# Optimization experiments

Hardware: AMD Instinct MI355X
Metric: run time of the kernel (lower is better)

## Reference

```python
import jax, jax.numpy as jnp
import numpy as np

K = 16  # knn


def conv1x1(x, w, b):
    # x: (B,Cin,k,N), w: (Cout,Cin), b: (Cout,)
    return jnp.einsum('oc,bckn->bokn', w, x) + b[None, :, None, None]


def leaky(x):
    return jnp.where(x >= 0, x, 0.2 * x)


def conv_res(x, sc_w, sc_b, a_w, a_b, b_w, b_b, c_w, c_b):
    sc = conv1x1(x, sc_w, sc_b)
    h = leaky(conv1x1(x, a_w, a_b))
    h = leaky(conv1x1(h, b_w, b_b))
    h = conv1x1(h, c_w, c_b)
    return h + sc


def get_knn_feature(xyz, k):
    # xyz: (B,3,N) -> feature (B,10,k,N)
    x_t = jnp.transpose(xyz, (0, 2, 1))  # (B,N,3)
    xx = jnp.sum(x_t * x_t, axis=-1)  # (B,N)
    inner = jnp.einsum('bnc,bmc->bnm', x_t, x_t)  # (B,N,N)
    d2 = xx[:, :, None] + xx[:, None, :] - 2.0 * inner  # squared dists
    _, idx = jax.lax.top_k(-d2, k)  # (B,N,k) nearest (includes self)
    neighbors = jax.vmap(lambda pts, i: pts[i])(x_t, idx)  # (B,N,k,3)
    center = x_t[:, :, None, :]  # (B,N,1,3)
    rel = neighbors - center
    dist = jnp.sqrt(jnp.sum(rel * rel, axis=-1, keepdims=True) + 1e-12)  # (B,N,k,1)
    feat = jnp.concatenate([jnp.broadcast_to(center, neighbors.shape), neighbors, rel, dist], axis=-1)  # (B,N,k,10)
    return jnp.transpose(feat, (0, 3, 2, 1))  # (B,10,k,N)


def _mk_w(key, o, i):
    s = 1.0 / np.sqrt(i)
    return jax.random.uniform(key, (o, i), jnp.float32, -s, s)


def setup_inputs():
    key = jax.random.key(0)
    ks = jax.random.split(key, 20)
    B, N = 4, 8192
    hide, out = 64, 128
    inp = {'xyz': jax.random.normal(ks[0], (B, 3, N), jnp.float32)}
    # CONV_Res(10, 64, 64)
    inp['p1_sc_w'] = _mk_w(ks[1], hide, 10); inp['p1_sc_b'] = jnp.zeros((hide,), jnp.float32)
    inp['p1_a_w'] = _mk_w(ks[2], hide, 10); inp['p1_a_b'] = jnp.zeros((hide,), jnp.float32)
    inp['p1_b_w'] = _mk_w(ks[3], hide, hide); inp['p1_b_b'] = jnp.zeros((hide,), jnp.float32)
    inp['p1_c_w'] = _mk_w(ks[4], hide, hide); inp['p1_c_b'] = jnp.zeros((hide,), jnp.float32)
    # CONV_Res(128, 64, 128)
    inp['p2_sc_w'] = _mk_w(ks[5], out, 2 * hide); inp['p2_sc_b'] = jnp.zeros((out,), jnp.float32)
    inp['p2_a_w'] = _mk_w(ks[6], hide, 2 * hide); inp['p2_a_b'] = jnp.zeros((hide,), jnp.float32)
    inp['p2_b_w'] = _mk_w(ks[7], out, hide); inp['p2_b_b'] = jnp.zeros((out,), jnp.float32)
    inp['p2_c_w'] = _mk_w(ks[8], out, out); inp['p2_c_b'] = jnp.zeros((out,), jnp.float32)
    return inp


def reference(xyz, p1_sc_w, p1_sc_b, p1_a_w, p1_a_b, p1_b_w, p1_b_b, p1_c_w, p1_c_b,
              p2_sc_w, p2_sc_b, p2_a_w, p2_a_b, p2_b_w, p2_b_b, p2_c_w, p2_c_b):
    x = get_knn_feature(xyz, K)  # (B,10,k,N)
    x = conv_res(x, p1_sc_w, p1_sc_b, p1_a_w, p1_a_b, p1_b_w, p1_b_b, p1_c_w, p1_c_b)  # (B,64,k,N)
    x1 = jnp.max(x, axis=2, keepdims=True)  # (B,64,1,N)
    x1 = jnp.broadcast_to(x1, x.shape)  # repeat over k
    x = jnp.concatenate([x, x1], axis=1)  # (B,128,k,N)
    x = conv_res(x, p2_sc_w, p2_sc_b, p2_a_w, p2_a_b, p2_b_w, p2_b_b, p2_c_w, p2_c_b)  # (B,128,k,N)
    return jnp.max(x, axis=2)  # (B,128,N)
```

## Files before the change

kernel.cpp:

```cpp
#include <hip/hip_runtime.h>
#include <hip/hip_bf16.h>

#define B_ 4
#define N_ 8192
#define KNN 16
#define BN_ (B_*N_)
#define NPOS (BN_*KNN)

typedef __attribute__((ext_vector_type(8))) short bf16x8;
typedef __attribute__((ext_vector_type(4))) float f32x4;

static __device__ __forceinline__ unsigned short f2bf(float f) {
  union { float f; unsigned u; } v; v.f = f;
  unsigned r = v.u + 0x7fff + ((v.u >> 16) & 1);
  return (unsigned short)(r >> 16);
}
static __device__ __forceinline__ float lk(float x) { return x >= 0.f ? x : 0.2f*x; }
static __device__ __forceinline__ unsigned pk2(float a, float b) {
  return (unsigned)f2bf(a) | ((unsigned)f2bf(b) << 16);
}

__global__ void k_prep(const float* __restrict__ xyz, float4* __restrict__ pts4) {
  int i = blockIdx.x * 256 + threadIdx.x;
  if (i >= BN_) return;
  int b = i >> 13, n = i & (N_-1);
  const float* p = xyz + b*3*N_;
  float x = p[n], y = p[N_+n], z = p[2*N_+n];
  float xx = fmaf(z, z, fmaf(y, y, x*x));
  pts4[i] = make_float4(x, y, z, xx);
}

__global__ void k_wcvt(const float* __restrict__ w_sc, const float* __restrict__ w_a,
                       const float* __restrict__ w_b, const float* __restrict__ w_c,
                       const float* __restrict__ p1a, const float* __restrict__ p1sc,
                       const float* __restrict__ p1b, const float* __restrict__ p1c,
                       unsigned short* __restrict__ out) {
  int i = blockIdx.x*256 + threadIdx.x;
  if (i >= 61440) return;
  if (i < 49152) {
    int x = i*2;
    const float* w; int base, K2;
    if (x < 32768)      { w = w_sc; base = 0;     K2 = 256; }
    else if (x < 49152) { w = w_a;  base = 32768; K2 = 256; }
    else if (x < 65536) { w = w_b;  base = 49152; K2 = 128; }
    else                { w = w_c;  base = 65536; K2 = 256; }
    int off = x - base;
    int row = off / K2;
    int colb = (off & (K2-1)) ^ ((row & 7) << 4);
    int k = colb >> 1;
    out[i] = f2bf(w[row*(K2 >> 1) + k]);
  } else {
    int e = i - 49152;
    float val; int byteoff;
    if (e < 2048) {
      int row = e >> 5, k = e & 31;
      val = (k < 10) ? p1a[row*10 + k] : 0.f;
      byteoff = row*64 + ((2*k) ^ ((row & 3) << 4));
    } else if (e < 4096) {
      int le = e - 2048, row = le >> 5, k = le & 31;
      val = (k < 10) ? p1sc[row*10 + k] : 0.f;
      byteoff = 4096 + row*64 + ((2*k) ^ ((row & 3) << 4));
    } else if (e < 8192) {
      int le = e - 4096, row = le >> 6, k = le & 63;
      val = p1b[row*64 + k];
      byteoff = 8192 + row*128 + ((2*k) ^ ((row & 7) << 4));
    } else {
      int le = e - 8192, row = le >> 6, k = le & 63;
      val = p1c[row*64 + k];
      byteoff = 16384 + row*128 + ((2*k) ^ ((row & 7) << 4));
    }
    out[49152 + (byteoff >> 1)] = f2bf(val);
  }
}

static __device__ __forceinline__ unsigned long long bitonic64(
    unsigned long long key, int lane) {
  #pragma unroll
  for (int size = 2; size <= 64; size <<= 1) {
    #pragma unroll
    for (int stride = size >> 1; stride >= 1; stride >>= 1) {
      unsigned long long ok = __shfl_xor((long long)key, stride);
      bool up = ((lane & size) == 0);
      bool keepmin = (((lane & stride) == 0) == up);
      bool oless = ok < key;
      if (oless == keepmin) key = ok;
    }
  }
  return key;
}

template<int U>
static __device__ __forceinline__ void scan_groups(
    const float4* __restrict__ cand, int itbase, int ch,
    float4 me, int lane,
    unsigned long long* __restrict__ bw,
    unsigned long long& topk, float& rhs, int& cnt) {
  float s[U]; int cid[U];
  #pragma unroll
  for (int u = 0; u < U; ++u) {
    int ci = (itbase + u)*64 + lane;
    float4 c = cand[ci];
    float dot = fmaf(me.z, c.z, fmaf(me.y, c.y, me.x*c.x));
    s[u] = fmaf(-2.0f, dot, c.w);
    cid[u] = ch*2048 + ci;
  }
  #pragma unroll
  for (int u = 0; u < U; ++u) {
    unsigned long long m = __ballot(s[u] < rhs);
    if (m) {
      int prefix = __builtin_amdgcn_mbcnt_hi((unsigned)(m >> 32),
                    __builtin_amdgcn_mbcnt_lo((unsigned)m, 0));
      if (s[u] < rhs) {
        float d2 = me.w + s[u];
        bw[cnt + prefix] =
          ((unsigned long long)__float_as_uint(d2) << 32) | (unsigned)cid[u];
      }
      cnt += __popcll(m);
      if (cnt >= 48) {
        int base = 0;
        while (cnt > 0) {
          int c2 = cnt > 48 ? 48 : cnt;
          unsigned long long e = (lane < 16) ? topk
            : ((lane - 16) < c2 ? bw[base + lane - 16] : ~0ull);
          topk = bitonic64(e, lane);
          base += c2; cnt -= c2;
        }
        unsigned long long k15 = __shfl((long long)topk, 15);
        rhs = __uint_as_float((unsigned)(k15 >> 32)) - me.w;
      }
    }
  }
}

__global__ __launch_bounds__(512) void k_knn(const float4* __restrict__ pts4,
                                             int* __restrict__ knn) {
  __shared__ float4 cand[2048];
  __shared__ unsigned long long buf[8][112];
  const int lane = threadIdx.x & 63;
  const int wv   = threadIdx.x >> 6;
  const int q = blockIdx.x * 8 + wv;
  const int b = q >> 13;
  const int n = q & (N_-1);
  const float4* __restrict__ P = pts4 + (b << 13);
  float4 me = P[n];

  unsigned long long topk = ~0ull;
  float rhs = __builtin_inff();
  int cnt = 0;
  unsigned long long* __restrict__ bw = buf[wv];

  for (int ch = 0; ch < 4; ++ch) {
    __syncthreads();
    #pragma unroll
    for (int t = 0; t < 4; ++t)
      cand[t*512 + threadIdx.x] = P[ch*2048 + t*512 + threadIdx.x];
    __syncthreads();

    if (ch == 0) {
      float4 c = cand[lane];
      float dot = fmaf(me.z, c.z, fmaf(me.y, c.y, me.x*c.x));
      float d2 = (me.w + c.w) - 2.0f*dot;
      unsigned long long key =
        ((unsigned long long)__float_as_uint(d2) << 32) | (unsigned)lane;
      topk = bitonic64(key, lane);
      unsigned long long k15 = __shfl((long long)topk, 15);
      rhs = __uint_as_float((unsigned)(k15 >> 32)) - me.w;
      scan_groups<3>(cand, 1, 0, me, lane, bw, topk, rhs, cnt);
      #pragma unroll 1
      for (int it = 4; it < 32; it += 4)
        scan_groups<4>(cand, it, 0, me, lane, bw, topk, rhs, cnt);
    } else {
      #pragma unroll 1
      for (int it = 0; it < 32; it += 4)
        scan_groups<4>(cand, it, ch, me, lane, bw, topk, rhs, cnt);
    }
  }
  {
    int base = 0;
    while (cnt > 0) {
      int c2 = cnt > 48 ? 48 : cnt;
      unsigned long long e = (lane < 16) ? topk
        : ((lane - 16) < c2 ? bw[base + lane - 16] : ~0ull);
      topk = bitonic64(e, lane);
      base += c2; cnt -= c2;
    }
  }
  if (lane < 16) knn[(q << 4) + lane] = (int)(unsigned)(topk & 0xffffffffu);
}

__global__ __launch_bounds__(512, 4) void k_p1(
    const float4* __restrict__ pts4, const int* __restrict__ knn,
    const unsigned short* __restrict__ wbf,
    const float* __restrict__ a_b, const float* __restrict__ b_b,
    const float* __restrict__ c_b, const float* __restrict__ sc_b,
    unsigned short* __restrict__ X, unsigned short* __restrict__ XM) {
  __shared__ __align__(16) unsigned short Ws1[12288];
  __shared__ __align__(16) unsigned short Fs[8192];
  __shared__ __align__(16) unsigned short Hr[16384];
  const int tid = threadIdx.x;
  const int lane = tid & 63, wv = tid >> 6;
  const int colr = lane & 15, kq = lane >> 4;

  #pragma unroll
  for (int j = 0; j < 3; ++j) {
    int c = j*512 + tid;
    ((uint4*)Ws1)[c] = ((const uint4*)(wbf + 49152))[c];
  }
  const char* WS = (const char*)Ws1;
  char* H = (char*)Hr + wv*4096;

  for (int tile = 0; tile < 4; ++tile) {
    const int bn0 = (blockIdx.x*4 + tile) * 16;
    __syncthreads();
    if (tid < 256) {
      int bnl = tid >> 4, kk = tid & 15;
      int bn = bn0 + bnl;
      int b = bn >> 13;
      float4 cp = pts4[bn];
      int nid = knn[bn*16 + kk];
      float4 np = pts4[(b << 13) + nid];
      float rx = np.x - cp.x, ry = np.y - cp.y, rz = np.z - cp.z;
      float dist = sqrtf(fmaf(rz, rz, fmaf(ry, ry, rx*rx)) + 1e-12f);
      unsigned short row[32];
      row[0]=f2bf(cp.x); row[1]=f2bf(cp.y); row[2]=f2bf(cp.z);
      row[3]=f2bf(np.x); row[4]=f2bf(np.y); row[5]=f2bf(np.z);
      row[6]=f2bf(rx);   row[7]=f2bf(ry);   row[8]=f2bf(rz);   row[9]=f2bf(dist);
      #pragma unroll
      for (int j = 10; j < 32; ++j) row[j] = 0;
      int wvp = tid >> 5, posl = tid & 31;
      char* dst = (char*)Fs + wvp*2048 + posl*64;
      #pragma unroll
      for (int c = 0; c < 4; ++c)
        *(uint4*)(dst + ((c*16) ^ ((posl&3)<<4))) = *(const uint4*)(row + c*8);
    }
    __syncthreads();

    bf16x8 bfr[2];
    #pragma unroll
    for (int ct = 0; ct < 2; ++ct) {
      int posl = ct*16 + colr;
      bfr[ct] = *(const bf16x8*)((const char*)Fs + wv*2048 + posl*64 + ((kq*16) ^ ((posl&3)<<4)));
    }

    f32x4 acc[4][2];
    #pragma unroll
    for (int mt = 0; mt < 4; ++mt) {
      int r0 = mt*16 + kq*4;
      #pragma unroll
      for (int r = 0; r < 4; ++r) {
        float bia = c_b[r0+r] + sc_b[r0+r];
        acc[mt][0][r] = bia; acc[mt][1][r] = bia;
      }
    }
    #pragma unroll
    for (int mt = 0; mt < 4; ++mt) {
      int row = mt*16 + colr;
      bf16x8 w = *(const bf16x8*)(WS + 4096 + row*64 + ((kq*16) ^ ((row&3)<<4)));
      acc[mt][0] = __builtin_amdgcn_mfma_f32_16x16x32_bf16(w, bfr[0], acc[mt][0], 0, 0, 0);
      acc[mt][1] = __builtin_amdgcn_mfma_f32_16x16x32_bf16(w, bfr[1], acc[mt][1], 0, 0, 0);
    }

    f32x4 ha[4][2];
    #pragma unroll
    for (int mt = 0; mt < 4; ++mt) {
      int r0 = mt*16 + kq*4;
      #pragma unroll
      for (int r = 0; r < 4; ++r) { ha[mt][0][r] = a_b[r0+r]; ha[mt][1][r] = a_b[r0+r]; }
    }
    #pragma unroll
    for (int mt = 0; mt < 4; ++mt) {
      int row = mt*16 + colr;
      bf16x8 w = *(const bf16x8*)(WS + row*64 + ((kq*16) ^ ((row&3)<<4)));
      ha[mt][0] = __builtin_amdgcn_mfma_f32_16x16x32_bf16(w, bfr[0], ha[mt][0], 0, 0, 0);
      ha[mt][1] = __builtin_amdgcn_mfma_f32_16x16x32_bf16(w, bfr[1], ha[mt][1], 0, 0, 0);
    }

    #pragma unroll
    for (int mt = 0; mt < 4; ++mt) {
      int ch2 = (mt*16 + kq*4) * 2;
      #pragma unroll
      for (int ct = 0; ct < 2; ++ct) {
        int posl = ct*16 + colr;
        uint2 u;
        u.x = pk2(lk(ha[mt][ct][0]), lk(ha[mt][ct][1]));
        u.y = pk2(lk(ha[mt][ct][2]), lk(ha[mt][ct][3]));
        *(uint2*)(H + posl*128 + (ch2 ^ ((posl&7)<<4))) = u;
      }
    }
    bf16x8 bh[2][2];
    #pragma unroll
    for (int ct = 0; ct < 2; ++ct) {
      int posl = ct*16 + colr;
      #pragma unroll
      for (int k2 = 0; k2 < 2; ++k2)
        bh[ct][k2] = *(const bf16x8*)(H + posl*128 + ((k2*64 + kq*16) ^ ((posl&7)<<4)));
    }

    #pragma unroll
    for (int jj = 0; jj < 2; ++jj) {
      f32x4 h2[2][2];
      #pragma unroll
      for (int mtp = 0; mtp < 2; ++mtp) {
        int r0 = (jj*2 + mtp)*16 + kq*4;
        #pragma unroll
        for (int r = 0; r < 4; ++r) { h2[mtp][0][r] = b_b[r0+r]; h2[mtp][1][r] = b_b[r0+r]; }
      }
      #pragma unroll
      for (int mtp = 0; mtp < 2; ++mtp) {
        int row = (jj*2 + mtp)*16 + colr;
        #pragma unroll
        for (int k2 = 0; k2 < 2; ++k2) {
          bf16x8 w = *(const bf16x8*)(WS + 8192 + row*128 + ((k2*64 + kq*16) ^ ((row&7)<<4)));
          h2[mtp][0] = __builtin_amdgcn_mfma_f32_16x16x32_bf16(w, bh[0][k2], h2[mtp][0], 0, 0, 0);
          h2[mtp][1] = __builtin_amdgcn_mfma_f32_16x16x32_bf16(w, bh[1][k2], h2[mtp][1], 0, 0, 0);
        }
      }
      #pragma unroll
      for (int mtp = 0; mtp < 2; ++mtp) {
        int ch2 = ((jj*2 + mtp)*16 + kq*4) * 2;
        #pragma unroll
        for (int ct = 0; ct < 2; ++ct) {
          int posl = ct*16 + colr;
          uint2 u;
          u.x = pk2(lk(h2[mtp][ct][0]), lk(h2[mtp][ct][1]));
          u.y = pk2(lk(h2[mtp][ct][2]), lk(h2[mtp][ct][3]));
          *(uint2*)(H + posl*128 + (ch2 ^ ((posl&7)<<4))) = u;
        }
      }
      bf16x8 b2[2];
      #pragma unroll
      for (int ct = 0; ct < 2; ++ct) {
        int posl = ct*16 + colr;
        b2[ct] = *(const bf16x8*)(H + posl*128 + ((jj*64 + kq*16) ^ ((posl&7)<<4)));
      }
      #pragma unroll
      for (int mt = 0; mt < 4; ++mt) {
        int row = mt*16 + colr;
        bf16x8 w = *(const bf16x8*)(WS + 16384 + row*128 + ((jj*64 + kq*16) ^ ((row&7)<<4)));
        acc[mt][0] = __builtin_amdgcn_mfma_f32_16x16x32_bf16(w, b2[0], acc[mt][0], 0, 0, 0);
        acc[mt][1] = __builtin_amdgcn_mfma_f32_16x16x32_bf16(w, b2[1], acc[mt][1], 0, 0, 0);
      }
    }

    #pragma unroll
    for (int ct = 0; ct < 2; ++ct) {
      int bn = bn0 + wv*2 + ct;
      #pragma unroll
      for (int mt = 0; mt < 4; ++mt) {
        int ch0 = mt*16 + kq*4;
        uint2 u;
        u.x = pk2(acc[mt][ct][0], acc[mt][ct][1]);
        u.y = pk2(acc[mt][ct][2], acc[mt][ct][3]);
        *(uint2*)(X + ((size_t)(bn*16 + colr))*64 + ch0) = u;
        float m[4];
        #pragma unroll
        for (int r = 0; r < 4; ++r) {
          float v = acc[mt][ct][r];
          v = fmaxf(v, __shfl_xor(v, 1));
          v = fmaxf(v, __shfl_xor(v, 2));
          v = fmaxf(v, __shfl_xor(v, 4));
          v = fmaxf(v, __shfl_xor(v, 8));
          m[r] = v;
        }
        if (colr == 0) {
          uint2 um; um.x = pk2(m[0], m[1]); um.y = pk2(m[2], m[3]);
          *(uint2*)(XM + (size_t)bn*64 + ch0) = um;
        }
      }
    }
  }
}

struct P2Shared {
  unsigned short Ws[49152];
  unsigned short Hr[8][2048];
  float outT[128][16];
};

static __device__ __forceinline__ void p2_loadbx(
    bf16x8 (&dst)[2][4], const unsigned short* __restrict__ X,
    const unsigned short* __restrict__ XM, int bn0, int wv, int colr, int kq) {
  #pragma unroll
  for (int ct = 0; ct < 2; ++ct) {
    int bn = bn0 + wv*2 + ct;
    const unsigned short* xr = X + ((size_t)bn*16 + colr)*64 + kq*8;
    dst[ct][0] = *(const bf16x8*)(xr);
    dst[ct][1] = *(const bf16x8*)(xr + 32);
    const unsigned short* mr = XM + (size_t)bn*64 + kq*8;
    dst[ct][2] = *(const bf16x8*)(mr);
    dst[ct][3] = *(const bf16x8*)(mr + 32);
  }
}

__global__ __launch_bounds__(512, 2) void k_p2(
    const unsigned short* __restrict__ X, const unsigned short* __restrict__ XM,
    const unsigned short* __restrict__ wbf,
    const float* __restrict__ sc_b, const float* __restrict__ a_b,
    const float* __restrict__ b_b, const float* __restrict__ c_b,
    float* __restrict__ out) {
  __shared__ __align__(16) P2Shared S;
  const int tid = threadIdx.x;
  const int lane = tid & 63, wv = tid >> 6;
  const int colr = lane & 15, kq = lane >> 4;

  #pragma unroll
  for (int it = 0; it < 12; ++it) {
    int c = it*512 + tid;
    *(uint4*)((char*)S.Ws + c*16) = *(const uint4*)((const char*)wbf + c*16);
  }

  const char* WSC = (const char*)S.Ws;
  const char* WA  = (const char*)(S.Ws + 16384);
  const char* WB  = (const char*)(S.Ws + 24576);
  const char* WC  = (const char*)(S.Ws + 32768);
  char* H = (char*)S.Hr[wv];

#define WF(base, row, K2, ksbyte) \
  (*(const bf16x8*)((base) + (row)*(K2) + ((((ksbyte) + kq*16)) ^ (((row)&7)<<4))))

  bf16x8 bx[2][4], bxn[2][4];
  p2_loadbx(bx, X, XM, blockIdx.x*8*16, wv, colr, kq);
  __syncthreads();

  for (int t = 0; t < 8; ++t) {
    const int bn0 = (blockIdx.x*8 + t) * 16;

    f32x4 acc[8][2];
    #pragma unroll
    for (int mt = 0; mt < 8; ++mt) {
      int r0 = mt*16 + kq*4;
      #pragma unroll
      for (int r = 0; r < 4; ++r) {
        float bia = c_b[r0+r] + sc_b[r0+r];
        acc[mt][0][r] = bia; acc[mt][1][r] = bia;
      }
    }
    #pragma unroll
    for (int mt = 0; mt < 8; ++mt) {
      int row = mt*16 + colr;
      #pragma unroll
      for (int ks = 0; ks < 4; ++ks) {
        bf16x8 w = WF(WSC, row, 256, ks*64);
        acc[mt][0] = __builtin_amdgcn_mfma_f32_16x16x32_bf16(w, bx[0][ks], acc[mt][0], 0, 0, 0);
        acc[mt][1] = __builtin_amdgcn_mfma_f32_16x16x32_bf16(w, bx[1][ks], acc[mt][1], 0, 0, 0);
      }
    }

    f32x4 ha[4][2];
    #pragma unroll
    for (int mt = 0; mt < 4; ++mt) {
      int r0 = mt*16 + kq*4;
      #pragma unroll
      for (int r = 0; r < 4; ++r) { ha[mt][0][r] = a_b[r0+r]; ha[mt][1][r] = a_b[r0+r]; }
    }
    #pragma unroll
    for (int mt = 0; mt < 4; ++mt) {
      int row = mt*16 + colr;
      #pragma unroll
      for (int ks = 0; ks < 4; ++ks) {
        bf16x8 w = WF(WA, row, 256, ks*64);
        ha[mt][0] = __builtin_amdgcn_mfma_f32_16x16x32_bf16(w, bx[0][ks], ha[mt][0], 0, 0, 0);
        ha[mt][1] = __builtin_amdgcn_mfma_f32_16x16x32_bf16(w, bx[1][ks], ha[mt][1], 0, 0, 0);
      }
    }

    {
      int tn = (t < 7) ? (t + 1) : 7;
      p2_loadbx(bxn, X, XM, (blockIdx.x*8 + tn) * 16, wv, colr, kq);
    }

    #pragma unroll
    for (int mt = 0; mt < 4; ++mt) {
      int ch2 = (mt*16 + kq*4) * 2;
      #pragma unroll
      for (int ct = 0; ct < 2; ++ct) {
        int posl = ct*16 + colr;
        uint2 u;
        u.x = pk2(lk(ha[mt][ct][0]), lk(ha[mt][ct][1]));
        u.y = pk2(lk(ha[mt][ct][2]), lk(ha[mt][ct][3]));
        *(uint2*)(H + posl*128 + (ch2 ^ ((posl&7)<<4))) = u;
      }
    }
    bf16x8 bh[2][2];
    #pragma unroll
    for (int ct = 0; ct < 2; ++ct) {
      int posl = ct*16 + colr;
      #pragma unroll
      for (int k2 = 0; k2 < 2; ++k2)
        bh[ct][k2] = *(const bf16x8*)(H + posl*128 + ((k2*64 + kq*16) ^ ((posl&7)<<4)));
    }

    #pragma unroll
    for (int j = 0; j < 4; ++j) {
      f32x4 h2[2][2];
      #pragma unroll
      for (int mtp = 0; mtp < 2; ++mtp) {
        int r0 = (2*j + mtp)*16 + kq*4;
        #pragma unroll
        for (int r = 0; r < 4; ++r) { h2[mtp][0][r] = b_b[r0+r]; h2[mtp][1][r] = b_b[r0+r]; }
      }
      #pragma unroll
      for (int mtp = 0; mtp < 2; ++mtp) {
        int row = (2*j + mtp)*16 + colr;
        #pragma unroll
        for (int k2 = 0; k2 < 2; ++k2) {
          bf16x8 w = WF(WB, row, 128, k2*64);
          h2[mtp][0] = __builtin_amdgcn_mfma_f32_16x16x32_bf16(w, bh[0][k2], h2[mtp][0], 0, 0, 0);
          h2[mtp][1] = __builtin_amdgcn_mfma_f32_16x16x32_bf16(w, bh[1][k2], h2[mtp][1], 0, 0, 0);
        }
      }
      char* PB = H + (j & 1)*2048;
      #pragma unroll
      for (int mtp = 0; mtp < 2; ++mtp) {
        int chp2 = (mtp*16 + kq*4) * 2;
        #pragma unroll
        for (int ct = 0; ct < 2; ++ct) {
          int posl = ct*16 + colr;
          uint2 u;
          u.x = pk2(lk(h2[mtp][ct][0]), lk(h2[mtp][ct][1]));
          u.y = pk2(lk(h2[mtp][ct][2]), lk(h2[mtp][ct][3]));
          *(uint2*)(PB + posl*64 + (chp2 ^ ((posl&3)<<4))) = u;
        }
      }
      bf16x8 b2[2];
      #pragma unroll
      for (int ct = 0; ct < 2; ++ct) {
        int posl = ct*16 + colr;
        b2[ct] = *(const bf16x8*)(PB + posl*64 + ((kq*16) ^ ((posl&3)<<4)));
      }
      #pragma unroll
      for (int mt = 0; mt < 8; ++mt) {
        int row = mt*16 + colr;
        bf16x8 w = WF(WC, row, 256, j*64);
        acc[mt][0] = __builtin_amdgcn_mfma_f32_16x16x32_bf16(w, b2[0], acc[mt][0], 0, 0, 0);
        acc[mt][1] = __builtin_amdgcn_mfma_f32_16x16x32_bf16(w, b2[1], acc[mt][1], 0, 0, 0);
      }
    }

    __syncthreads();
    #pragma unroll
    for (int mt = 0; mt < 8; ++mt) {
      #pragma unroll
      for (int ct = 0; ct < 2; ++ct) {
        #pragma unroll
        for (int r = 0; r < 4; ++r) {
          float v = acc[mt][ct][r];
          v = fmaxf(v, __shfl_xor(v, 1));
          v = fmaxf(v, __shfl_xor(v, 2));
          v = fmaxf(v, __shfl_xor(v, 4));
          v = fmaxf(v, __shfl_xor(v, 8));
          if (colr == 0) S.outT[mt*16 + kq*4 + r][wv*2 + ct] = v;
        }
      }
    }
    __syncthreads();
    {
      int ch = tid >> 2, p = tid & 3;
      int b = bn0 >> 13, n0 = bn0 & (N_-1);
      float4 v4 = *(const float4*)&S.outT[ch][p*4];
      *(float4*)(out + ((size_t)b*128 + ch)*N_ + n0 + p*4) = v4;
    }

    #pragma unroll
    for (int ct = 0; ct < 2; ++ct)
      #pragma unroll
      for (int ks = 0; ks < 4; ++ks)
        bx[ct][ks] = bxn[ct][ks];
  }
#undef WF
}

extern "C" void kernel_launch(void* const* d_in, const int* in_sizes, int n_in,
                              void* d_out, int out_size, void* d_ws, size_t ws_size,
                              hipStream_t stream) {
  const float* xyz     = (const float*)d_in[0];
  const float* p1_sc_w = (const float*)d_in[1];
  const float* p1_sc_b = (const float*)d_in[2];
  const float* p1_a_w  = (const float*)d_in[3];
  const float* p1_a_b  = (const float*)d_in[4];
  const float* p1_b_w  = (const float*)d_in[5];
  const float* p1_b_b  = (const float*)d_in[6];
  const float* p1_c_w  = (const float*)d_in[7];
  const float* p1_c_b  = (const float*)d_in[8];
  const float* p2_sc_w = (const float*)d_in[9];
  const float* p2_sc_b = (const float*)d_in[10];
  const float* p2_a_w  = (const float*)d_in[11];
  const float* p2_a_b  = (const float*)d_in[12];
  const float* p2_b_w  = (const float*)d_in[13];
  const float* p2_b_b  = (const float*)d_in[14];
  const float* p2_c_w  = (const float*)d_in[15];
  const float* p2_c_b  = (const float*)d_in[16];

  if (ws_size < 75497472u) return;
  char* ws = (char*)d_ws;
  float4* pts4        = (float4*)(ws);
  unsigned short* wbf = (unsigned short*)(ws + 524288);
  int* knn            = (int*)(ws + 655360);
  unsigned short* X   = (unsigned short*)(ws + 4194304);
  unsigned short* XM  = (unsigned short*)(ws + 4194304 + 67108864);
  float* out = (float*)d_out;

  k_prep<<<dim3(BN_/256), dim3(256), 0, stream>>>(xyz, pts4);
  k_wcvt<<<dim3(240), dim3(256), 0, stream>>>(p2_sc_w, p2_a_w, p2_b_w, p2_c_w,
      p1_a_w, p1_sc_w, p1_b_w, p1_c_w, wbf);
  k_knn<<<dim3(BN_/8), dim3(512), 0, stream>>>(pts4, knn);
  k_p1<<<dim3(512), dim3(512), 0, stream>>>(pts4, knn, wbf,
      p1_a_b, p1_b_b, p1_c_b, p1_sc_b, X, XM);
  k_p2<<<dim3(256), dim3(512), 0, stream>>>(X, XM, wbf,
      p2_sc_b, p2_a_b, p2_b_b, p2_c_b, out);
}
```

Baseline: 377.7 us.

## Fuse stage-1 and stage-2 conv-res kernels, keeping intermediates in shared memory

Merges the first conv-res block, the k-max, and the second conv-res block into one kernel. The bf16 intermediate X/XM tensors now stay in per-wave LDS instead of making a round trip through global memory. Each lane now builds its MFMA input fragment directly in registers, which drops the shared feature staging buffer and one barrier. The cost is that both weight sets live in LDS and register pressure rises, which lowers occupancy (launch bounds go to 2 blocks per CU). The prefetch of the next tile's inputs that the old stage-2 kernel used is also lost.

New measurement: 379.5 us. No clear change (+0.5%).

```diff
diff --git a/kernel.cpp b/kernel.cpp
--- a/kernel.cpp
+++ b/kernel.cpp
@@ -188,76 +188,87 @@
   if (lane < 16) knn[(q << 4) + lane] = (int)(unsigned)(topk & 0xffffffffu);
 }
 
-__global__ __launch_bounds__(512, 4) void k_p1(
+__global__ __launch_bounds__(512, 2) void k_p12(
     const float4* __restrict__ pts4, const int* __restrict__ knn,
     const unsigned short* __restrict__ wbf,
-    const float* __restrict__ a_b, const float* __restrict__ b_b,
-    const float* __restrict__ c_b, const float* __restrict__ sc_b,
-    unsigned short* __restrict__ X, unsigned short* __restrict__ XM) {
+    const float* __restrict__ a_b1, const float* __restrict__ b_b1,
+    const float* __restrict__ c_b1, const float* __restrict__ sc_b1,
+    const float* __restrict__ sc_b2, const float* __restrict__ a_b2,
+    const float* __restrict__ b_b2, const float* __restrict__ c_b2,
+    float* __restrict__ out) {
   __shared__ __align__(16) unsigned short Ws1[12288];
-  __shared__ __align__(16) unsigned short Fs[8192];
-  __shared__ __align__(16) unsigned short Hr[16384];
+  __shared__ __align__(16) unsigned short Ws2[49152];
+  __shared__ __align__(16) unsigned short Hr[8][2304];
   const int tid = threadIdx.x;
   const int lane = tid & 63, wv = tid >> 6;
   const int colr = lane & 15, kq = lane >> 4;
 
   #pragma unroll
-  for (int j = 0; j < 3; ++j) {
-    int c = j*512 + tid;
-    ((uint4*)Ws1)[c] = ((const uint4*)(wbf + 49152))[c];
-  }
+  for (int j = 0; j < 3; ++j)
+    ((uint4*)Ws1)[j*512 + tid] = ((const uint4*)(wbf + 49152))[j*512 + tid];
+  #pragma unroll
+  for (int it = 0; it < 12; ++it)
+    ((uint4*)Ws2)[it*512 + tid] = ((const uint4*)wbf)[it*512 + tid];
+
   const char* WS = (const char*)Ws1;
-  char* H = (char*)Hr + wv*4096;
-
-  for (int tile = 0; tile < 4; ++tile) {
-    const int bn0 = (blockIdx.x*4 + tile) * 16;
-    __syncthreads();
-    if (tid < 256) {
-      int bnl = tid >> 4, kk = tid & 15;
-      int bn = bn0 + bnl;
+  const char* WSC = (const char*)Ws2;
+  const char* WA  = (const char*)(Ws2 + 16384);
+  const char* WB  = (const char*)(Ws2 + 24576);
+  const char* WC  = (const char*)(Ws2 + 32768);
+  char* H = (char*)Hr[wv];
+  float (*outT)[16] = (float(*)[16])(&Hr[0][0]);
+
+#define WF(base, row, K2, ksbyte) \
+  (*(const bf16x8*)((base) + (row)*(K2) + ((((ksbyte) + kq*16)) ^ (((row)&7)<<4))))
+
+  __syncthreads();
+
+  for (int t = 0; t < 8; ++t) {
+    const int bn0 = blockIdx.x*128 + t*16;
+
+    unsigned short fb0[10], fb1[10];
+    #pragma unroll
+    for (int ct = 0; ct < 2; ++ct) {
+      int bn = bn0 + wv*2 + ct;
       int b = bn >> 13;
       float4 cp = pts4[bn];
-      int nid = knn[bn*16 + kk];
+      int nid = knn[bn*16 + colr];
       float4 np = pts4[(b << 13) + nid];
       float rx = np.x - cp.x, ry = np.y - cp.y, rz = np.z - cp.z;
       float dist = sqrtf(fmaf(rz, rz, fmaf(ry, ry, rx*rx)) + 1e-12f);
-      unsigned short row[32];
-      row[0]=f2bf(cp.x); row[1]=f2bf(cp.y); row[2]=f2bf(cp.z);
-      row[3]=f2bf(np.x); row[4]=f2bf(np.y); row[5]=f2bf(np.z);
-      row[6]=f2bf(rx);   row[7]=f2bf(ry);   row[8]=f2bf(rz);   row[9]=f2bf(dist);
-      #pragma unroll
-      for (int j = 10; j < 32; ++j) row[j] = 0;
-      int wvp = tid >> 5, posl = tid & 31;
-      char* dst = (char*)Fs + wvp*2048 + posl*64;
-      #pragma unroll
-      for (int c = 0; c < 4; ++c)
-        *(uint4*)(dst + ((c*16) ^ ((posl&3)<<4))) = *(const uint4*)(row + c*8);
-    }
-    __syncthreads();
-
+      unsigned short* fb = ct ? fb1 : fb0;
+      fb[0]=f2bf(cp.x); fb[1]=f2bf(cp.y); fb[2]=f2bf(cp.z);
+      fb[3]=f2bf(np.x); fb[4]=f2bf(np.y); fb[5]=f2bf(np.z);
+      fb[6]=f2bf(rx);   fb[7]=f2bf(ry);   fb[8]=f2bf(rz);   fb[9]=f2bf(dist);
+    }
     bf16x8 bfr[2];
     #pragma unroll
     for (int ct = 0; ct < 2; ++ct) {
-      int posl = ct*16 + colr;
-      bfr[ct] = *(const bf16x8*)((const char*)Fs + wv*2048 + posl*64 + ((kq*16) ^ ((posl&3)<<4)));
-    }
-
-    f32x4 acc[4][2];
+      const unsigned short* fb = ct ? fb1 : fb0;
+      #pragma unroll
+      for (int j = 0; j < 8; ++j) {
+        unsigned short v1 = (j < 2) ? fb[8+j] : (unsigned short)0;
+        unsigned short e = (kq == 0) ? fb[j] : ((kq == 1) ? v1 : (unsigned short)0);
+        bfr[ct][j] = (short)e;
+      }
+    }
+
+    f32x4 acc1[4][2];
     #pragma unroll
     for (int mt = 0; mt < 4; ++mt) {
       int r0 = mt*16 + kq*4;
       #pragma unroll
       for (int r = 0; r < 4; ++r) {
-        float bia = c_b[r0+r] + sc_b[r0+r];
-        acc[mt][0][r] = bia; acc[mt][1][r] = bia;
+        float bia = c_b1[r0+r] + sc_b1[r0+r];
+        acc1[mt][0][r] = bia; acc1[mt][1][r] = bia;
       }
     }
     #pragma unroll
     for (int mt = 0; mt < 4; ++mt) {
       int row = mt*16 + colr;
       bf16x8 w = *(const bf16x8*)(WS + 4096 + row*64 + ((kq*16) ^ ((row&3)<<4)));
-      acc[mt][0] = __builtin_amdgcn_mfma_f32_16x16x32_bf16(w, bfr[0], acc[mt][0], 0, 0, 0);
-      acc[mt][1] = __builtin_amdgcn_mfma_f32_16x16x32_bf16(w, bfr[1], acc[mt][1], 0, 0, 0);
+      acc1[mt][0] = __builtin_amdgcn_mfma_f32_16x16x32_bf16(w, bfr[0], acc1[mt][0], 0, 0, 0);
+      acc1[mt][1] = __builtin_amdgcn_mfma_f32_16x16x32_bf16(w, bfr[1], acc1[mt][1], 0, 0, 0);
     }
 
     f32x4 ha[4][2];
@@ -265,7 +276,7 @@
     for (int mt = 0; mt < 4; ++mt) {
       int r0 = mt*16 + kq*4;
       #pragma unroll
-      for (int r = 0; r < 4; ++r) { ha[mt][0][r] = a_b[r0+r]; ha[mt][1][r] = a_b[r0+r]; }
+      for (int r = 0; r < 4; ++r) { ha[mt][0][r] = a_b1[r0+r]; ha[mt][1][r] = a_b1[r0+r]; }
     }
     #pragma unroll
     for (int mt = 0; mt < 4; ++mt) {
@@ -287,13 +298,13 @@
         *(uint2*)(H + posl*128 + (ch2 ^ ((posl&7)<<4))) = u;
       }
     }
-    bf16x8 bh[2][2];
+    bf16x8 bh1[2][2];
     #pragma unroll
     for (int ct = 0; ct < 2; ++ct) {
       int posl = ct*16 + colr;
       #pragma unroll
       for (int k2 = 0; k2 < 2; ++k2)
-        bh[ct][k2] = *(const bf16x8*)(H + posl*128 + ((k2*64 + kq*16) ^ ((posl&7)<<4)));
+        bh1[ct][k2] = *(const bf16x8*)(H + posl*128 + ((k2*64 + kq*16) ^ ((posl&7)<<4)));
     }
 
     #pragma unroll
@@ -303,7 +314,7 @@
       for (int mtp = 0; mtp < 2; ++mtp) {
         int r0 = (jj*2 + mtp)*16 + kq*4;
         #pragma unroll
-        for (int r = 0; r < 4; ++r) { h2[mtp][0][r] = b_b[r0+r]; h2[mtp][1][r] = b_b[r0+r]; }
+        for (int r = 0; r < 4; ++r) { h2[mtp][0][r] = b_b1[r0+r]; h2[mtp][1][r] = b_b1[r0+r]; }
       }
       #pragma unroll
       for (int mtp = 0; mtp < 2; ++mtp) {
@@ -311,8 +322,8 @@
         #pragma unroll
         for (int k2 = 0; k2 < 2; ++k2) {
           bf16x8 w = *(const bf16x8*)(WS + 8192 + row*128 + ((k2*64 + kq*16) ^ ((row&7)<<4)));
-          h2[mtp][0] = __builtin_amdgcn_mfma_f32_16x16x32_bf16(w, bh[0][k2], h2[mtp][0], 0, 0, 0);
-          h2[mtp][1] = __builtin_amdgcn_mfma_f32_16x16x32_bf16(w, bh[1][k2], h2[mtp][1], 0, 0, 0);
+          h2[mtp][0] = __builtin_amdgcn_mfma_f32_16x16x32_bf16(w, bh1[0][k2], h2[mtp][0], 0, 0, 0);
+          h2[mtp][1] = __builtin_amdgcn_mfma_f32_16x16x32_bf16(w, bh1[1][k2], h2[mtp][1], 0, 0, 0);
         }
       }
       #pragma unroll
@@ -337,22 +348,160 @@
       for (int mt = 0; mt < 4; ++mt) {
         int row = mt*16 + colr;
         bf16x8 w = *(const bf16x8*)(WS + 16384 + row*128 + ((jj*64 + kq*16) ^ ((row&7)<<4)));
-        acc[mt][0] = __builtin_amdgcn_mfma_f32_16x16x32_bf16(w, b2[0], acc[mt][0], 0, 0, 0);
-        acc[mt][1] = __builtin_amdgcn_mfma_f32_16x16x32_bf16(w, b2[1], acc[mt][1], 0, 0, 0);
+        acc1[mt][0] = __builtin_amdgcn_mfma_f32_16x16x32_bf16(w, b2[0], acc1[mt][0], 0, 0, 0);
+        acc1[mt][1] = __builtin_amdgcn_mfma_f32_16x16x32_bf16(w, b2[1], acc1[mt][1], 0, 0, 0);
       }
     }
 
     #pragma unroll
     for (int ct = 0; ct < 2; ++ct) {
-      int bn = bn0 + wv*2 + ct;
+      int posl = ct*16 + colr;
       #pragma unroll
       for (int mt = 0; mt < 4; ++mt) {
         int ch0 = mt*16 + kq*4;
         uint2 u;
-        u.x = pk2(acc[mt][ct][0], acc[mt][ct][1]);
-        u.y = pk2(acc[mt][ct][2], acc[mt][ct][3]);
-        *(uint2*)(X + ((size_t)(bn*16 + colr))*64 + ch0) = u;
+        u.x = pk2(acc1[mt][ct][0], acc1[mt][ct][1]);
+        u.y = pk2(acc1[mt][ct][2], acc1[mt][ct][3]);
+        *(uint2*)(H + ((posl*128 + ch0*2) ^ ((posl&7)<<4))) = u;
         float m[4];
+        #pragma unroll
+        for (int r = 0; r < 4; ++r) {
+          float v = acc1[mt][ct][r];
+          v = fmaxf(v, __shfl_xor(v, 1));
+          v = fmaxf(v, __shfl_xor(v, 2));
+          v = fmaxf(v, __shfl_xor(v, 4));
+          v = fmaxf(v, __shfl_xor(v, 8));
+          m[r] = v;
+        }
+        if (colr == 0) {
+          uint2 um; um.x = pk2(m[0], m[1]); um.y = pk2(m[2], m[3]);
+          *(uint2*)(H + 4096 + ct*128 + ch0*2) = um;
+        }
+      }
+    }
+
+    bf16x8 bx[2][4];
+    #pragma unroll
+    for (int ct = 0; ct < 2; ++ct) {
+      int posl = ct*16 + colr;
+      bx[ct][0] = *(const bf16x8*)(H + ((posl*128 + kq*16) ^ ((posl&7)<<4)));
+      bx[ct][1] = *(const bf16x8*)(H + ((posl*128 + 64 + kq*16) ^ ((posl&7)<<4)));
+      bx[ct][2] = *(const bf16x8*)(H + 4096 + ct*128 + kq*16);
+      bx[ct][3] = *(const bf16x8*)(H + 4096 + ct*128 + 64 + kq*16);
+    }
+
+    f32x4 acc[8][2];
+    #pragma unroll
+    for (int mt = 0; mt < 8; ++mt) {
+      int r0 = mt*16 + kq*4;
+      #pragma unroll
+      for (int r = 0; r < 4; ++r) {
+        float bia = c_b2[r0+r] + sc_b2[r0+r];
+        acc[mt][0][r] = bia; acc[mt][1][r] = bia;
+      }
+    }
+    #pragma unroll
+    for (int mt = 0; mt < 8; ++mt) {
+      int row = mt*16 + colr;
+      #pragma unroll
+      for (int ks = 0; ks < 4; ++ks) {
+        bf16x8 w = WF(WSC, row, 256, ks*64);
+        acc[mt][0] = __builtin_amdgcn_mfma_f32_16x16x32_bf16(w, bx[0][ks], acc[mt][0], 0, 0, 0);
+        acc[mt][1] = __builtin_amdgcn_mfma_f32_16x16x32_bf16(w, bx[1][ks], acc[mt][1], 0, 0, 0);
+      }
+    }
+
+    f32x4 ha2[4][2];
+    #pragma unroll
+    for (int mt = 0; mt < 4; ++mt) {
+      int r0 = mt*16 + kq*4;
+      #pragma unroll
+      for (int r = 0; r < 4; ++r) { ha2[mt][0][r] = a_b2[r0+r]; ha2[mt][1][r] = a_b2[r0+r]; }
+    }
+    #pragma unroll
+    for (int mt = 0; mt < 4; ++mt) {
+      int row = mt*16 + colr;
+      #pragma unroll
+      for (int ks = 0; ks < 4; ++ks) {
+        bf16x8 w = WF(WA, row, 256, ks*64);
+        ha2[mt][0] = __builtin_amdgcn_mfma_f32_16x16x32_bf16(w, bx[0][ks], ha2[mt][0], 0, 0, 0);
+        ha2[mt][1] = __builtin_amdgcn_mfma_f32_16x16x32_bf16(w, bx[1][ks], ha2[mt][1], 0, 0, 0);
+      }
+    }
+
+    #pragma unroll
+    for (int mt = 0; mt < 4; ++mt) {
+      int ch2 = (mt*16 + kq*4) * 2;
+      #pragma unroll
+      for (int ct = 0; ct < 2; ++ct) {
+        int posl = ct*16 + colr;
+        uint2 u;
+        u.x = pk2(lk(ha2[mt][ct][0]), lk(ha2[mt][ct][1]));
+        u.y = pk2(lk(ha2[mt][ct][2]), lk(ha2[mt][ct][3]));
+        *(uint2*)(H + posl*128 + (ch2 ^ ((posl&7)<<4))) = u;
+      }
+    }
+    bf16x8 bh[2][2];
+    #pragma unroll
+    for (int ct = 0; ct < 2; ++ct) {
+      int posl = ct*16 + colr;
+      #pragma unroll
+      for (int k2 = 0; k2 < 2; ++k2)
+        bh[ct][k2] = *(const bf16x8*)(H + posl*128 + ((k2*64 + kq*16) ^ ((posl&7)<<4)));
+    }
+
+    #pragma unroll
+    for (int j = 0; j < 4; ++j) {
+      f32x4 h2[2][2];
+      #pragma unroll
+      for (int mtp = 0; mtp < 2; ++mtp) {
+        int r0 = (2*j + mtp)*16 + kq*4;
+        #pragma unroll
+        for (int r = 0; r < 4; ++r) { h2[mtp][0][r] = b_b2[r0+r]; h2[mtp][1][r] = b_b2[r0+r]; }
+      }
+      #pragma unroll
+      for (int mtp = 0; mtp < 2; ++mtp) {
+        int row = (2*j + mtp)*16 + colr;
+        #pragma unroll
+        for (int k2 = 0; k2 < 2; ++k2) {
+          bf16x8 w = WF(WB, row, 128, k2*64);
+          h2[mtp][0] = __builtin_amdgcn_mfma_f32_16x16x32_bf16(w, bh[0][k2], h2[mtp][0], 0, 0, 0);
+          h2[mtp][1] = __builtin_amdgcn_mfma_f32_16x16x32_bf16(w, bh[1][k2], h2[mtp][1], 0, 0, 0);
+        }
+      }
+      char* PB = H + (j & 1)*2048;
+      #pragma unroll
+      for (int mtp = 0; mtp < 2; ++mtp) {
+        int chp2 = (mtp*16 + kq*4) * 2;
+        #pragma unroll
+        for (int ct = 0; ct < 2; ++ct) {
+          int posl = ct*16 + colr;
+          uint2 u;
+          u.x = pk2(lk(h2[mtp][ct][0]), lk(h2[mtp][ct][1]));
+          u.y = pk2(lk(h2[mtp][ct][2]), lk(h2[mtp][ct][3]));
+          *(uint2*)(PB + posl*64 + (chp2 ^ ((posl&3)<<4))) = u;
+        }
+      }
+      bf16x8 b2[2];
+      #pragma unroll
+      for (int ct = 0; ct < 2; ++ct) {
+        int posl = ct*16 + colr;
+        b2[ct] = *(const bf16x8*)(PB + posl*64 + ((kq*16) ^ ((posl&3)<<4)));
+      }
+      #pragma unroll
+      for (int mt = 0; mt < 8; ++mt) {
+        int row = mt*16 + colr;
+        bf16x8 w = WF(WC, row, 256, j*64);
+        acc[mt][0] = __builtin_amdgcn_mfma_f32_16x16x32_bf16(w, b2[0], acc[mt][0], 0, 0, 0);
+        acc[mt][1] = __builtin_amdgcn_mfma_f32_16x16x32_bf16(w, b2[1], acc[mt][1], 0, 0, 0);
+      }
+    }
+
+    __syncthreads();
+    #pragma unroll
+    for (int mt = 0; mt < 8; ++mt) {
+      #pragma unroll
+      for (int ct = 0; ct < 2; ++ct) {
         #pragma unroll
         for (int r = 0; r < 4; ++r) {
           float v = acc[mt][ct][r];
@@ -360,196 +509,7 @@
           v = fmaxf(v, __shfl_xor(v, 2));
           v = fmaxf(v, __shfl_xor(v, 4));
           v = fmaxf(v, __shfl_xor(v, 8));
-          m[r] = v;
-        }
-        if (colr == 0) {
-          uint2 um; um.x = pk2(m[0], m[1]); um.y = pk2(m[2], m[3]);
-          *(uint2*)(XM + (size_t)bn*64 + ch0) = um;
-        }
-      }
-    }
-  }
-}
-
-struct P2Shared {
-  unsigned short Ws[49152];
-  unsigned short Hr[8][2048];
-  float outT[128][16];
-};
-
-static __device__ __forceinline__ void p2_loadbx(
-    bf16x8 (&dst)[2][4], const unsigned short* __restrict__ X,
-    const unsigned short* __restrict__ XM, int bn0, int wv, int colr, int kq) {
-  #pragma unroll
-  for (int ct = 0; ct < 2; ++ct) {
-    int bn = bn0 + wv*2 + ct;
-    const unsigned short* xr = X + ((size_t)bn*16 + colr)*64 + kq*8;
-    dst[ct][0] = *(const bf16x8*)(xr);
-    dst[ct][1] = *(const bf16x8*)(xr + 32);
-    const unsigned short* mr = XM + (size_t)bn*64 + kq*8;
-    dst[ct][2] = *(const bf16x8*)(mr);
-    dst[ct][3] = *(const bf16x8*)(mr + 32);
-  }
-}
-
-__global__ __launch_bounds__(512, 2) void k_p2(
-    const unsigned short* __restrict__ X, const unsigned short* __restrict__ XM,
-    const unsigned short* __restrict__ wbf,
-    const float* __restrict__ sc_b, const float* __restrict__ a_b,
-    const float* __restrict__ b_b, const float* __restrict__ c_b,
-    float* __restrict__ out) {
-  __shared__ __align__(16) P2Shared S;
-  const int tid = threadIdx.x;
-  const int lane = tid & 63, wv = tid >> 6;
-  const int colr = lane & 15, kq = lane >> 4;
-
-  #pragma unroll
-  for (int it = 0; it < 12; ++it) {
-    int c = it*512 + tid;
-    *(uint4*)((char*)S.Ws + c*16) = *(const uint4*)((const char*)wbf + c*16);
-  }
-
-  const char* WSC = (const char*)S.Ws;
-  const char* WA  = (const char*)(S.Ws + 16384);
-  const char* WB  = (const char*)(S.Ws + 24576);
-  const char* WC  = (const char*)(S.Ws + 32768);
-  char* H = (char*)S.Hr[wv];
-
-#define WF(base, row, K2, ksbyte) \
-  (*(const bf16x8*)((base) + (row)*(K2) + ((((ksbyte) + kq*16)) ^ (((row)&7)<<4))))
-
-  bf16x8 bx[2][4], bxn[2][4];
-  p2_loadbx(bx, X, XM, blockIdx.x*8*16, wv, colr, kq);
-  __syncthreads();
-
-  for (int t = 0; t < 8; ++t) {
-    const int bn0 = (blockIdx.x*8 + t) * 16;
-
-    f32x4 acc[8][2];
-    #pragma unroll
-    for (int mt = 0; mt < 8; ++mt) {
-      int r0 = mt*16 + kq*4;
-      #pragma unroll
-      for (int r = 0; r < 4; ++r) {
-        float bia = c_b[r0+r] + sc_b[r0+r];
-        acc[mt][0][r] = bia; acc[mt][1][r] = bia;
-      }
-    }
-    #pragma unroll
-    for (int mt = 0; mt < 8; ++mt) {
-      int row = mt*16 + colr;
-      #pragma unroll
-      for (int ks = 0; ks < 4; ++ks) {
-        bf16x8 w = WF(WSC, row, 256, ks*64);
-        acc[mt][0] = __builtin_amdgcn_mfma_f32_16x16x32_bf16(w, bx[0][ks], acc[mt][0], 0, 0, 0);
-        acc[mt][1] = __builtin_amdgcn_mfma_f32_16x16x32_bf16(w, bx[1][ks], acc[mt][1], 0, 0, 0);
-      }
-    }
-
-    f32x4 ha[4][2];
-    #pragma unroll
-    for (int mt = 0; mt < 4; ++mt) {
-      int r0 = mt*16 + kq*4;
-      #pragma unroll
-      for (int r = 0; r < 4; ++r) { ha[mt][0][r] = a_b[r0+r]; ha[mt][1][r] = a_b[r0+r]; }
-    }
-    #pragma unroll
-    for (int mt = 0; mt < 4; ++mt) {
-      int row = mt*16 + colr;
-      #pragma unroll
-      for (int ks = 0; ks < 4; ++ks) {
-        bf16x8 w = WF(WA, row, 256, ks*64);
-        ha[mt][0] = __builtin_amdgcn_mfma_f32_16x16x32_bf16(w, bx[0][ks], ha[mt][0], 0, 0, 0);
-        ha[mt][1] = __builtin_amdgcn_mfma_f32_16x16x32_bf16(w, bx[1][ks], ha[mt][1], 0, 0, 0);
-      }
-    }
-
-    {
-      int tn = (t < 7) ? (t + 1) : 7;
-      p2_loadbx(bxn, X, XM, (blockIdx.x*8 + tn) * 16, wv, colr, kq);
-    }
-
-    #pragma unroll
-    for (int mt = 0; mt < 4; ++mt) {
-      int ch2 = (mt*16 + kq*4) * 2;
-      #pragma unroll
-      for (int ct = 0; ct < 2; ++ct) {
-        int posl = ct*16 + colr;
-        uint2 u;
-        u.x = pk2(lk(ha[mt][ct][0]), lk(ha[mt][ct][1]));
-        u.y = pk2(lk(ha[mt][ct][2]), lk(ha[mt][ct][3]));
-        *(uint2*)(H + posl*128 + (ch2 ^ ((posl&7)<<4))) = u;
-      }
-    }
-    bf16x8 bh[2][2];
-    #pragma unroll
-    for (int ct = 0; ct < 2; ++ct) {
-      int posl = ct*16 + colr;
-      #pragma unroll
-      for (int k2 = 0; k2 < 2; ++k2)
-        bh[ct][k2] = *(const bf16x8*)(H + posl*128 + ((k2*64 + kq*16) ^ ((posl&7)<<4)));
-    }
-
-    #pragma unroll
-    for (int j = 0; j < 4; ++j) {
-      f32x4 h2[2][2];
-      #pragma unroll
-      for (int mtp = 0; mtp < 2; ++mtp) {
-        int r0 = (2*j + mtp)*16 + kq*4;
-        #pragma unroll
-        for (int r = 0; r < 4; ++r) { h2[mtp][0][r] = b_b[r0+r]; h2[mtp][1][r] = b_b[r0+r]; }
-      }
-      #pragma unroll
-      for (int mtp = 0; mtp < 2; ++mtp) {
-        int row = (2*j + mtp)*16 + colr;
-        #pragma unroll
-        for (int k2 = 0; k2 < 2; ++k2) {
-          bf16x8 w = WF(WB, row, 128, k2*64);
-          h2[mtp][0] = __builtin_amdgcn_mfma_f32_16x16x32_bf16(w, bh[0][k2], h2[mtp][0], 0, 0, 0);
-          h2[mtp][1] = __builtin_amdgcn_mfma_f32_16x16x32_bf16(w, bh[1][k2], h2[mtp][1], 0, 0, 0);
-        }
-      }
-      char* PB = H + (j & 1)*2048;
-      #pragma unroll
-      for (int mtp = 0; mtp < 2; ++mtp) {
-        int chp2 = (mtp*16 + kq*4) * 2;
-        #pragma unroll
-        for (int ct = 0; ct < 2; ++ct) {
-          int posl = ct*16 + colr;
-          uint2 u;
-          u.x = pk2(lk(h2[mtp][ct][0]), lk(h2[mtp][ct][1]));
-          u.y = pk2(lk(h2[mtp][ct][2]), lk(h2[mtp][ct][3]));
-          *(uint2*)(PB + posl*64 + (chp2 ^ ((posl&3)<<4))) = u;
-        }
-      }
-      bf16x8 b2[2];
-      #pragma unroll
-      for (int ct = 0; ct < 2; ++ct) {
-        int posl = ct*16 + colr;
-        b2[ct] = *(const bf16x8*)(PB + posl*64 + ((kq*16) ^ ((posl&3)<<4)));
-      }
-      #pragma unroll
-      for (int mt = 0; mt < 8; ++mt) {
-        int row = mt*16 + colr;
-        bf16x8 w = WF(WC, row, 256, j*64);
-        acc[mt][0] = __builtin_amdgcn_mfma_f32_16x16x32_bf16(w, b2[0], acc[mt][0], 0, 0, 0);
-        acc[mt][1] = __builtin_amdgcn_mfma_f32_16x16x32_bf16(w, b2[1], acc[mt][1], 0, 0, 0);
-      }
-    }
-
-    __syncthreads();
-    #pragma unroll
-    for (int mt = 0; mt < 8; ++mt) {
-      #pragma unroll
-      for (int ct = 0; ct < 2; ++ct) {
-        #pragma unroll
-        for (int r = 0; r < 4; ++r) {
-          float v = acc[mt][ct][r];
-          v = fmaxf(v, __shfl_xor(v, 1));
-          v = fmaxf(v, __shfl_xor(v, 2));
-          v = fmaxf(v, __shfl_xor(v, 4));
-          v = fmaxf(v, __shfl_xor(v, 8));
-          if (colr == 0) S.outT[mt*16 + kq*4 + r][wv*2 + ct] = v;
+          if (colr == 0) outT[mt*16 + kq*4 + r][wv*2 + ct] = v;
         }
       }
     }
@@ -557,15 +517,10 @@
     {
       int ch = tid >> 2, p = tid & 3;
       int b = bn0 >> 13, n0 = bn0 & (N_-1);
-      float4 v4 = *(const float4*)&S.outT[ch][p*4];
+      float4 v4 = *(const float4*)&outT[ch][p*4];
       *(float4*)(out + ((size_t)b*128 + ch)*N_ + n0 + p*4) = v4;
     }
-
-    #pragma unroll
-    for (int ct = 0; ct < 2; ++ct)
-      #pragma unroll
-      for (int ks = 0; ks < 4; ++ks)
-        bx[ct][ks] = bxn[ct][ks];
+    __syncthreads();
   }
 #undef WF
 }
@@ -596,16 +551,13 @@
   float4* pts4        = (float4*)(ws);
   unsigned short* wbf = (unsigned short*)(ws + 524288);
   int* knn            = (int*)(ws + 655360);
-  unsigned short* X   = (unsigned short*)(ws + 4194304);
-  unsigned short* XM  = (unsigned short*)(ws + 4194304 + 67108864);
   float* out = (float*)d_out;
 
   k_prep<<<dim3(BN_/256), dim3(256), 0, stream>>>(xyz, pts4);
   k_wcvt<<<dim3(240), dim3(256), 0, stream>>>(p2_sc_w, p2_a_w, p2_b_w, p2_c_w,
       p1_a_w, p1_sc_w, p1_b_w, p1_c_w, wbf);
   k_knn<<<dim3(BN_/8), dim3(512), 0, stream>>>(pts4, knn);
-  k_p1<<<dim3(512), dim3(512), 0, stream>>>(pts4, knn, wbf,
-      p1_a_b, p1_b_b, p1_c_b, p1_sc_b, X, XM);
-  k_p2<<<dim3(256), dim3(512), 0, stream>>>(X, XM, wbf,
+  k_p12<<<dim3(256), dim3(512), 0, stream>>>(pts4, knn, wbf,
+      p1_a_b, p1_b_b, p1_c_b, p1_sc_b,
       p2_sc_b, p2_a_b, p2_b_b, p2_c_b, out);
 }
```
